# Performance work log

Measured on AMD Instinct MI355X. Metric: run time of the kernel, lower is better.

## Reference

```python
import jax, jax.numpy as jnp
import numpy as np

B, S, HID = 2, 2048, 1024
NH, HD = 4, 256
SCALE = HD ** -0.5


def _rope(x, fr, fi):
    # x: [B,S,NH,HD]; fr/fi: [S,HD//2]
    b, s, n, d = x.shape
    xr = x.reshape(b, s, n, d // 2, 2)
    re, im = xr[..., 0], xr[..., 1]
    fr = fr[None, :, None, :]
    fi = fi[None, :, None, :]
    rr = re * fr - im * fi
    ri = re * fi + im * fr
    return jnp.stack((rr, ri), axis=-1).reshape(b, s, n, d)


def setup_inputs() -> dict:
    key = jax.random.key(0)
    k1, k2, k3 = jax.random.split(key, 3)
    hidden_states = jax.random.normal(k1, (B, S, HID), dtype=jnp.float32)
    # RoPE frequencies (standard theta=10000)
    inv_freq = 1.0 / (10000.0 ** (np.arange(0, HD, 2, dtype=np.float32) / HD))  # [HD//2]
    t = np.arange(S, dtype=np.float32)
    ang = np.outer(t, inv_freq)  # [S, HD//2]
    freqs_real = jnp.asarray(np.cos(ang), dtype=jnp.float32)
    freqs_imag = jnp.asarray(np.sin(ang), dtype=jnp.float32)
    # causal additive mask [1,1,S,S]
    causal = jnp.tril(jnp.ones((S, S), dtype=bool))
    mask = jnp.where(causal, 0.0, -1e9).astype(jnp.float32)[None, None]
    W_qkv = jax.random.normal(k2, (3 * HID, HID), dtype=jnp.float32) * (HID ** -0.5)
    W_o = jax.random.normal(k3, (HID, HID), dtype=jnp.float32) * (HID ** -0.5)
    return {"hidden_states": hidden_states, "freqs_real": freqs_real,
            "freqs_imag": freqs_imag, "mask": mask, "W_qkv": W_qkv, "W_o": W_o}


def reference(hidden_states, freqs_real, freqs_imag, mask, W_qkv, W_o):
    b, s, _ = hidden_states.shape
    qkv = hidden_states @ W_qkv.T  # [B,S,3*HID]
    qkv = qkv.reshape(b, s, 3, NH, HD)
    q, k, v = qkv[:, :, 0], qkv[:, :, 1], qkv[:, :, 2]
    q = _rope(q, freqs_real, freqs_imag)
    k = _rope(k, freqs_real, freqs_imag)
    scores = jnp.einsum('bqhd,bkhd->bhqk', q * SCALE, k) + mask  # [B,NH,S,S]
    probs = jax.nn.softmax(scores, axis=-1)
    attn = jnp.einsum('bhqk,bkhd->bqhd', probs, v).reshape(b, s, HID)
    return attn @ W_o.T
```

## Files before the change

### kernel.cpp

```cpp
#include <hip/hip_runtime.h>
#include <stdint.h>

#define NB 2
#define NS 2048
#define NHID 1024
#define NHEADS 4
#define DHEAD 256
#define NP 128
#define QK_SCALE 0.0625f

typedef unsigned short ushort_t;
typedef __bf16 bf16x8 __attribute__((ext_vector_type(8)));
typedef float floatx4 __attribute__((ext_vector_type(4)));
typedef short shortx8 __attribute__((ext_vector_type(8)));
typedef unsigned short ushortx4 __attribute__((ext_vector_type(4)));
typedef unsigned short ushortx8 __attribute__((ext_vector_type(8)));

__device__ __forceinline__ float bf2f(ushort_t u) {
    unsigned int x = ((unsigned int)u) << 16;
    return __builtin_bit_cast(float, x);
}
__device__ __forceinline__ ushort_t f2bf(float f) {
    unsigned int u = __builtin_bit_cast(unsigned int, f);
    u += 0x7fff + ((u >> 16) & 1);
    return (ushort_t)(u >> 16);
}

__device__ __forceinline__ floatx4 mfma16(bf16x8 a, bf16x8 b, floatx4 c) {
    return __builtin_amdgcn_mfma_f32_16x16x32_bf16(a, b, c, 0, 0, 0);
}

__device__ __forceinline__ void gload_lds16(const void* g, void* l) {
    __builtin_amdgcn_global_load_lds(
        (const __attribute__((address_space(1))) void*)g,
        (__attribute__((address_space(3))) void*)l, 16, 0, 0);
}

#define N4_H (4096 * 1024 / 4)
#define N4_WQ (3072 * 1024 / 4)
#define N4_WO (1024 * 1024 / 4)
__global__ __launch_bounds__(256) void cast3_kernel(const float* __restrict__ inH,
                                                    const float* __restrict__ inWq,
                                                    const float* __restrict__ inWo,
                                                    ushort_t* __restrict__ out) {
    int i = blockIdx.x * 256 + threadIdx.x;
    const float* src;
    int j = i;
    if (i < N4_H) {
        src = inH;
    } else if (i < N4_H + N4_WQ) {
        src = inWq; j = i - N4_H;
    } else {
        src = inWo; j = i - (N4_H + N4_WQ);
    }
    float4 v = ((const float4*)src)[j];
    ushortx4 o = { f2bf(v.x), f2bf(v.y), f2bf(v.z), f2bf(v.w) };
    ((ushortx4*)out)[i] = o;
}


__global__ __launch_bounds__(256) void gemm_bt_f32s(const ushort_t* __restrict__ A,
                                                    const ushort_t* __restrict__ Bt,
                                                    float* __restrict__ C0,
                                                    float* __restrict__ C1,
                                                    int M, int N, int K) {
    __shared__ ushort_t sA[128 * 64];
    __shared__ ushort_t sB[128 * 64];
    const int t = threadIdx.x;
    const int m0 = blockIdx.y * 128;
    const int n0 = blockIdx.x * 128;
    const int kz = blockIdx.z;
    float* Cout = kz ? C1 : C0;
    const int kbeg = kz * (K / 2), kend = kbeg + K / 2;
    const int w = t >> 6, l = t & 63;
    const int wm = (w >> 1) * 64, wn = (w & 1) * 64;
    const int lc = l & 15, lq = l >> 4;

    floatx4 acc[4][4];
#pragma unroll
    for (int i = 0; i < 4; i++)
#pragma unroll
        for (int j = 0; j < 4; j++) acc[i][j] = (floatx4){0.f, 0.f, 0.f, 0.f};

    const int srow = w * 8 + (l >> 3);
    const int scol = ((((l & 7) - (l >> 3)) & 7)) * 8;
    const ushort_t* Ag = A + (size_t)(m0 + srow) * K + scol;
    const ushort_t* Bg = Bt + (size_t)(n0 + srow) * K + scol;
    ushort_t* lA = &sA[(size_t)t * 8];
    ushort_t* lB = &sB[(size_t)t * 8];

    for (int kk = kbeg; kk < kend; kk += 64) {
        __syncthreads();
#pragma unroll
        for (int j = 0; j < 4; j++) {
            gload_lds16(Ag + kk + (size_t)j * 32 * K, lA + j * 2048);
            gload_lds16(Bg + kk + (size_t)j * 32 * K, lB + j * 2048);
        }
        __syncthreads();
#pragma unroll
        for (int ks = 0; ks < 2; ks++) {
            bf16x8 af[4], bfv[4];
#pragma unroll
            for (int i = 0; i < 4; i++) {
                int R = wm + i * 16 + lc;
                af[i] = *(const bf16x8*)&sA[R * 64 + ((ks * 4 + lq + R) & 7) * 8];
            }
#pragma unroll
            for (int j = 0; j < 4; j++) {
                int R = wn + j * 16 + lc;
                bfv[j] = *(const bf16x8*)&sB[R * 64 + ((ks * 4 + lq + R) & 7) * 8];
            }
#pragma unroll
            for (int i = 0; i < 4; i++)
#pragma unroll
                for (int j = 0; j < 4; j++)
                    acc[i][j] = mfma16(af[i], bfv[j], acc[i][j]);
        }
    }

#pragma unroll
    for (int i = 0; i < 4; i++) {
        int row = m0 + wm + i * 16 + lq * 4;
#pragma unroll
        for (int j = 0; j < 4; j++) {
            int col = n0 + wn + j * 16 + lc;
#pragma unroll
            for (int r = 0; r < 4; r++)
                Cout[(size_t)(row + r) * N + col] = acc[i][j][r];
        }
    }
}

__global__ __launch_bounds__(256) void add_f32(const float* __restrict__ a,
                                               const float* __restrict__ b,
                                               float* __restrict__ o, int n4) {
    int i = blockIdx.x * 256 + threadIdx.x;
    if (i < n4) {
        float4 x = ((const float4*)a)[i];
        float4 y = ((const float4*)b)[i];
        float4 z = { x.x + y.x, x.y + y.y, x.z + y.z, x.w + y.w };
        ((float4*)o)[i] = z;
    }
}

__global__ __launch_bounds__(256) void gemm_qkv(const ushort_t* __restrict__ A,
                                                const ushort_t* __restrict__ Bt,
                                                const float* __restrict__ fre,
                                                const float* __restrict__ fim,
                                                ushort_t* __restrict__ Q,
                                                ushort_t* __restrict__ Kk,
                                                ushort_t* __restrict__ Vt) {
    const int M_K = 1024;
    __shared__ ushort_t sA[128 * 64];
    __shared__ ushort_t sB[128 * 64];
    const int t = threadIdx.x;
    const int m0 = blockIdx.y * 128;
    const int n0 = blockIdx.x * 128;
    const int w = t >> 6, l = t & 63;
    const int wm = (w >> 1) * 64, wn = (w & 1) * 64;
    const int lc = l & 15, lq = l >> 4;

    floatx4 acc[4][4];
#pragma unroll
    for (int i = 0; i < 4; i++)
#pragma unroll
        for (int j = 0; j < 4; j++) acc[i][j] = (floatx4){0.f, 0.f, 0.f, 0.f};

    const int srow = w * 8 + (l >> 3);
    const int scol = ((((l & 7) - (l >> 3)) & 7)) * 8;
    const ushort_t* Ag = A + (size_t)(m0 + srow) * M_K + scol;
    const ushort_t* Bg = Bt + (size_t)(n0 + srow) * M_K + scol;
    ushort_t* lA = &sA[(size_t)t * 8];
    ushort_t* lB = &sB[(size_t)t * 8];

    for (int kk = 0; kk < M_K; kk += 64) {
        __syncthreads();
#pragma unroll
        for (int j = 0; j < 4; j++) {
            gload_lds16(Ag + kk + (size_t)j * 32 * M_K, lA + j * 2048);
            gload_lds16(Bg + kk + (size_t)j * 32 * M_K, lB + j * 2048);
        }
        __syncthreads();
#pragma unroll
        for (int ks = 0; ks < 2; ks++) {
            bf16x8 af[4], bfv[4];
#pragma unroll
            for (int i = 0; i < 4; i++) {
                int R = wm + i * 16 + lc;
                af[i] = *(const bf16x8*)&sA[R * 64 + ((ks * 4 + lq + R) & 7) * 8];
            }
#pragma unroll
            for (int j = 0; j < 4; j++) {
                int R = wn + j * 16 + lc;
                bfv[j] = *(const bf16x8*)&sB[R * 64 + ((ks * 4 + lq + R) & 7) * 8];
            }
#pragma unroll
            for (int i = 0; i < 4; i++)
#pragma unroll
                for (int j = 0; j < 4; j++)
                    acc[i][j] = mfma16(af[i], bfv[j], acc[i][j]);
        }
    }

    const int sect = n0 >> 10;
#pragma unroll
    for (int i = 0; i < 4; i++) {
        int row = m0 + wm + i * 16 + lq * 4;
        int b = row >> 11;
        int srow2 = row & 2047;
#pragma unroll
        for (int j = 0; j < 4; j++) {
            int col = n0 + wn + j * 16 + lc;
            int d = col & 255;
            int h = (col >> 8) & 3;
            int bh = b * NHEADS + h;
            if (sect == 2) {
                ushortx4 pack = { f2bf(acc[i][j][0]), f2bf(acc[i][j][1]),
                                  f2bf(acc[i][j][2]), f2bf(acc[i][j][3]) };
                *(ushortx4*)&Vt[((size_t)bh * 256 + d) * NS + srow2] = pack;
            } else {
                int p = d >> 1;
                int odd = d & 1;
                ushort_t* dst = (sect == 0) ? Q : Kk;
#pragma unroll
                for (int r = 0; r < 4; r++) {
                    float v = acc[i][j][r];
                    float vp = __shfl_xor(v, 1);
                    int s = srow2 + r;
                    float c = fre[s * NP + p], si = fim[s * NP + p];
                    float out = odd ? (vp * si + v * c) : (v * c - vp * si);
                    if (sect == 0) out *= QK_SCALE;
                    dst[((size_t)bh * NS + s) * DHEAD + d] = f2bf(out);
                }
            }
        }
    }
}

#define BQ3 128
#define BKV3 64
#define PPAD 72
#define CHCAP 6
#define NPART_BH 51
#define OPART_SPLIT 224

__global__ __launch_bounds__(256, 2) void flash_attn4(const ushort_t* __restrict__ Q,
                                                      const ushort_t* __restrict__ K,
                                                      const ushort_t* __restrict__ Vt,
                                                      ushort_t* __restrict__ OpA,
                                                      ushort_t* __restrict__ OpB,
                                                      float* __restrict__ ml) {
    __shared__ ushort_t sK[BKV3 * 256];
    __shared__ ushort_t sV[DHEAD * 64];
    __shared__ ushort_t sP[4][16 * PPAD];

    int rem = blockIdx.x, qt = 15, nsp;
    for (;;) {
        nsp = (2 * (qt + 1) + CHCAP - 1) / CHCAP;
        if (rem < nsp) break;
        rem -= nsp;
        qt--;
    }
    const int nch = 2 * (qt + 1);
    const int cbeg = rem * CHCAP;
    const int cend = (cbeg + CHCAP < nch) ? cbeg + CHCAP : nch;

    const int h = blockIdx.y, b = blockIdx.z;
    const int t = threadIdx.x, w = t >> 6, l = t & 63;
    const int lc = l & 15, lq = l >> 4;
    const int bh = b * NHEADS + h;
    const size_t base = (size_t)bh * NS * DHEAD;
    const int q0 = qt * BQ3;

    const int krb = w * 2 + (l >> 5);
    const int kck = ((l & 31) - (krb & 7)) & 31;
    const size_t koff = (size_t)krb * 256 + kck * 8;
    const int vrb = w * 8 + (l >> 3);
    const int vck = ((l & 7) - (vrb & 7)) & 7;
    const size_t voff = (size_t)vrb * NS + vck * 8;
    ushort_t* dK = &sK[w * 512 + l * 8];
    ushort_t* dV = &sV[w * 512 + l * 8];

    bf16x8 qf[2][8];
#pragma unroll
    for (int gq = 0; gq < 2; gq++) {
        const ushort_t* qrow = Q + base + (size_t)(q0 + w * 32 + gq * 16 + lc) * DHEAD + lq * 8;
#pragma unroll
        for (int dk = 0; dk < 8; dk++) qf[gq][dk] = *(const bf16x8*)(qrow + dk * 32);
    }

    floatx4 accO[2][16];
#pragma unroll
    for (int gq = 0; gq < 2; gq++)
#pragma unroll
        for (int j = 0; j < 16; j++) accO[gq][j] = (floatx4){0.f, 0.f, 0.f, 0.f};
    float lrun[2][4] = {{0.f, 0.f, 0.f, 0.f}, {0.f, 0.f, 0.f, 0.f}};

    for (int kc = cbeg; kc < cend; kc++) {
        const int kb = kc * BKV3;
        __syncthreads();
        {
            const ushort_t* ksrc = K + base + (size_t)kb * 256 + koff;
            const ushort_t* vsrc = Vt + base + kb + voff;
#pragma unroll
            for (int j = 0; j < 8; j++)
                gload_lds16(ksrc + j * (8 * 256), dK + j * 2048);
#pragma unroll
            for (int j = 0; j < 8; j++)
                gload_lds16(vsrc + j * (32 * NS), dV + j * 2048);
        }
        __syncthreads();

        floatx4 sfr[2][4];
#pragma unroll
        for (int gq = 0; gq < 2; gq++)
#pragma unroll
            for (int g = 0; g < 4; g++) sfr[gq][g] = (floatx4){0.f, 0.f, 0.f, 0.f};
#pragma unroll
        for (int dk = 0; dk < 8; dk++) {
#pragma unroll
            for (int g = 0; g < 4; g++) {
                int R = g * 16 + lc;
                int phys = (dk * 4 + lq + (R & 7)) & 31;
                bf16x8 bk = *(const bf16x8*)&sK[R * 256 + phys * 8];
                sfr[0][g] = mfma16(qf[0][dk], bk, sfr[0][g]);
                sfr[1][g] = mfma16(qf[1][dk], bk, sfr[1][g]);
            }
        }

        if (kc >= nch - 2) {
#pragma unroll
            for (int gq = 0; gq < 2; gq++)
#pragma unroll
                for (int g = 0; g < 4; g++) {
                    int kg = kb + g * 16 + lc;
                    int qr = q0 + w * 32 + gq * 16 + lq * 4;
#pragma unroll
                    for (int r = 0; r < 4; r++)
                        if (kg > qr + r) sfr[gq][g][r] = -1e30f;
                }
        }

        ushort_t* pw = sP[w];
#pragma unroll
        for (int gq = 0; gq < 2; gq++) {
#pragma unroll
            for (int g = 0; g < 4; g++)
#pragma unroll
                for (int r = 0; r < 4; r++) {
                    float p = __expf(sfr[gq][g][r]);
                    lrun[gq][r] += p;
                    pw[(lq * 4 + r) * PPAD + g * 16 + lc] = f2bf(p);
                }
            bf16x8 ap0 = *(const bf16x8*)&pw[lc * PPAD + lq * 8];
            bf16x8 ap1 = *(const bf16x8*)&pw[lc * PPAD + 32 + lq * 8];
#pragma unroll
            for (int j = 0; j < 16; j++) {
                int D = j * 16 + lc;
                int ph0 = (lq + (D & 7)) & 7;
                int ph1 = (4 + lq + (D & 7)) & 7;
                bf16x8 bv0 = *(const bf16x8*)&sV[D * 64 + ph0 * 8];
                bf16x8 bv1 = *(const bf16x8*)&sV[D * 64 + ph1 * 8];
                accO[gq][j] = mfma16(ap0, bv0, accO[gq][j]);
                accO[gq][j] = mfma16(ap1, bv1, accO[gq][j]);
            }
        }
    }

    const int pid = bh * NPART_BH + blockIdx.x;
    ushort_t* op = (pid < OPART_SPLIT) ? OpA + (size_t)pid * (128 * 256)
                                       : OpB + (size_t)(pid - OPART_SPLIT) * (128 * 256);
#pragma unroll
    for (int gq = 0; gq < 2; gq++) {
#pragma unroll
        for (int r = 0; r < 4; r++) {
            int row = w * 32 + gq * 16 + lq * 4 + r;
#pragma unroll
            for (int j = 0; j < 16; j++)
                op[row * 256 + j * 16 + lc] = f2bf(accO[gq][j][r]);
            float lv = lrun[gq][r];
#pragma unroll
            for (int off = 1; off < 16; off <<= 1) lv += __shfl_xor(lv, off);
            if (lc == 0) ml[(size_t)pid * 128 + row] = lv;
        }
    }
}

__global__ __launch_bounds__(256) void combine_parts2(const ushort_t* __restrict__ OpA,
                                                      const ushort_t* __restrict__ OpB,
                                                      const float* __restrict__ ml,
                                                      ushort_t* __restrict__ O) {
    const int qt = blockIdx.x >> 3, rsub = blockIdx.x & 7;
    const int h = blockIdx.y, b = blockIdx.z;
    const int bh = b * NHEADS + h;
    int bbase = 0;
    for (int q = 15; q > qt; q--) bbase += (2 * (q + 1) + CHCAP - 1) / CHCAP;
    const int nsp = (2 * (qt + 1) + CHCAP - 1) / CHCAP;
    const int pid0 = bh * NPART_BH + bbase;

    const int t = threadIdx.x;
    const int rl = t >> 4;
    const int c0 = (t & 15) * 16;
    const int row = rsub * 16 + rl;

    float so[16];
#pragma unroll
    for (int k = 0; k < 16; k++) so[k] = 0.f;
    float sl = 0.f;

    for (int i = 0; i < nsp; i++) {
        int pid = pid0 + i;
        const ushort_t* op = (pid < OPART_SPLIT)
                                 ? OpA + (size_t)pid * (128 * 256)
                                 : OpB + (size_t)(pid - OPART_SPLIT) * (128 * 256);
        const ushort_t* p = op + row * 256 + c0;
        ushortx8 a0 = *(const ushortx8*)p;
        ushortx8 a1 = *(const ushortx8*)(p + 8);
#pragma unroll
        for (int k = 0; k < 8; k++) {
            so[k] += bf2f(a0[k]);
            so[8 + k] += bf2f(a1[k]);
        }
        sl += ml[(size_t)pid * 128 + row];
    }

    float inv = 1.f / sl;
    ushortx8 o0, o1;
#pragma unroll
    for (int k = 0; k < 8; k++) {
        o0[k] = f2bf(so[k] * inv);
        o1[k] = f2bf(so[8 + k] * inv);
    }
    int s = qt * BQ3 + row;
    ushort_t* dst = O + ((size_t)(b * NS + s) * NHEADS + h) * DHEAD + c0;
    *(ushortx8*)dst = o0;
    *(ushortx8*)(dst + 8) = o1;
}

extern "C" void kernel_launch(void* const* d_in, const int* in_sizes, int n_in,
                              void* d_out, int out_size, void* d_ws, size_t ws_size,
                              hipStream_t stream) {
    const float* hidden = (const float*)d_in[0];
    const float* fre = (const float*)d_in[1];
    const float* fim = (const float*)d_in[2];
    const float* Wqkv = (const float*)d_in[4];
    const float* Wo = (const float*)d_in[5];

    char* ws = (char*)d_ws;
    ushort_t* hb    = (ushort_t*)(ws);
    ushort_t* wqkvb = (ushort_t*)(ws + 8388608);
    ushort_t* wob   = (ushort_t*)(ws + 14680064);
    ushort_t* qb    = (ushort_t*)(ws + 16777216);
    ushort_t* kb    = (ushort_t*)(ws + 25165824);
    ushort_t* vtb   = (ushort_t*)(ws + 33554432);
    ushort_t* OpA   = (ushort_t*)(ws);
    ushort_t* OpB   = (ushort_t*)(ws + 41943040);
    ushort_t* oattn = (ushort_t*)(ws + 16777216);
    float*    gP0   = (float*)(ws + 25165824);
    float*    gP1   = (float*)(ws + 41943040);
    float*    ml    = (float*)(ws + 58720256);

    cast3_kernel<<<(N4_H + N4_WQ + N4_WO) / 256, 256, 0, stream>>>(hidden, Wqkv, Wo, hb);

    gemm_qkv<<<dim3(3072 / 128, 4096 / 128), 256, 0, stream>>>(
        hb, wqkvb, fre, fim, qb, kb, vtb);

    flash_attn4<<<dim3(NPART_BH, NHEADS, NB), 256, 0, stream>>>(qb, kb, vtb, OpA, OpB, ml);
    combine_parts2<<<dim3(128, NHEADS, NB), 256, 0, stream>>>(OpA, OpB, ml, oattn);

    gemm_bt_f32s<<<dim3(1024 / 128, 4096 / 128, 2), 256, 0, stream>>>(
        oattn, wob, gP0, gP1, 4096, 1024, 1024);
    add_f32<<<4096, 256, 0, stream>>>(gP0, gP1, (float*)d_out, 4096 * 1024 / 4);
}
```

Before: 208.6 us.

## Replace split-K output GEMM with 128x64 tiles and batch P·V over query groups

The output projection no longer splits K into two halves that write separate fp32 partial buffers and then need an add kernel. It now uses 128x64 tiles over the full K and writes directly to the output, which keeps the block count at 512 and drops one launch plus the partial-buffer traffic. In the attention kernel, the P tile for both 16-row query groups is stored in a swizzled 32x64 LDS layout, so each V fragment is loaded once and reused for both groups. This halves V reads from LDS, at the cost of more live registers and a longer K loop per GEMM block.

```diff
diff --git a/kernel.cpp b/kernel.cpp
--- a/kernel.cpp
+++ b/kernel.cpp
@@ -59,61 +59,60 @@
 }
 
 
-__global__ __launch_bounds__(256) void gemm_bt_f32s(const ushort_t* __restrict__ A,
+__global__ __launch_bounds__(256) void gemm_bt_f32n(const ushort_t* __restrict__ A,
                                                     const ushort_t* __restrict__ Bt,
-                                                    float* __restrict__ C0,
-                                                    float* __restrict__ C1,
+                                                    float* __restrict__ Cout,
                                                     int M, int N, int K) {
     __shared__ ushort_t sA[128 * 64];
-    __shared__ ushort_t sB[128 * 64];
+    __shared__ ushort_t sB[64 * 64];
     const int t = threadIdx.x;
     const int m0 = blockIdx.y * 128;
-    const int n0 = blockIdx.x * 128;
-    const int kz = blockIdx.z;
-    float* Cout = kz ? C1 : C0;
-    const int kbeg = kz * (K / 2), kend = kbeg + K / 2;
+    const int n0 = blockIdx.x * 64;
     const int w = t >> 6, l = t & 63;
-    const int wm = (w >> 1) * 64, wn = (w & 1) * 64;
+    const int wm = (w >> 1) * 64, wn = (w & 1) * 32;
     const int lc = l & 15, lq = l >> 4;
 
-    floatx4 acc[4][4];
+    floatx4 acc[4][2];
 #pragma unroll
     for (int i = 0; i < 4; i++)
 #pragma unroll
-        for (int j = 0; j < 4; j++) acc[i][j] = (floatx4){0.f, 0.f, 0.f, 0.f};
-
-    const int srow = w * 8 + (l >> 3);
-    const int scol = ((((l & 7) - (l >> 3)) & 7)) * 8;
-    const ushort_t* Ag = A + (size_t)(m0 + srow) * K + scol;
-    const ushort_t* Bg = Bt + (size_t)(n0 + srow) * K + scol;
+        for (int j = 0; j < 2; j++) acc[i][j] = (floatx4){0.f, 0.f, 0.f, 0.f};
+
+    const int arow = w * 8 + (l >> 3);
+    const int acol = (((l & 7) - (l >> 3)) & 7) * 8;
+    const ushort_t* Ag = A + (size_t)(m0 + arow) * K + acol;
     ushort_t* lA = &sA[(size_t)t * 8];
+    const int brow = t >> 3;
+    const int bcol = (((t & 7) - ((t >> 3) & 7)) & 7) * 8;
+    const ushort_t* Bg = Bt + (size_t)(n0 + brow) * K + bcol;
     ushort_t* lB = &sB[(size_t)t * 8];
 
-    for (int kk = kbeg; kk < kend; kk += 64) {
-        __syncthreads();
-#pragma unroll
-        for (int j = 0; j < 4; j++) {
+    for (int kk = 0; kk < K; kk += 64) {
+        __syncthreads();
+#pragma unroll
+        for (int j = 0; j < 4; j++)
             gload_lds16(Ag + kk + (size_t)j * 32 * K, lA + j * 2048);
+#pragma unroll
+        for (int j = 0; j < 2; j++)
             gload_lds16(Bg + kk + (size_t)j * 32 * K, lB + j * 2048);
-        }
         __syncthreads();
 #pragma unroll
         for (int ks = 0; ks < 2; ks++) {
-            bf16x8 af[4], bfv[4];
+            bf16x8 af[4], bfv[2];
 #pragma unroll
             for (int i = 0; i < 4; i++) {
                 int R = wm + i * 16 + lc;
                 af[i] = *(const bf16x8*)&sA[R * 64 + ((ks * 4 + lq + R) & 7) * 8];
             }
 #pragma unroll
-            for (int j = 0; j < 4; j++) {
+            for (int j = 0; j < 2; j++) {
                 int R = wn + j * 16 + lc;
                 bfv[j] = *(const bf16x8*)&sB[R * 64 + ((ks * 4 + lq + R) & 7) * 8];
             }
 #pragma unroll
             for (int i = 0; i < 4; i++)
 #pragma unroll
-                for (int j = 0; j < 4; j++)
+                for (int j = 0; j < 2; j++)
                     acc[i][j] = mfma16(af[i], bfv[j], acc[i][j]);
         }
     }
@@ -122,24 +121,12 @@
     for (int i = 0; i < 4; i++) {
         int row = m0 + wm + i * 16 + lq * 4;
 #pragma unroll
-        for (int j = 0; j < 4; j++) {
+        for (int j = 0; j < 2; j++) {
             int col = n0 + wn + j * 16 + lc;
 #pragma unroll
             for (int r = 0; r < 4; r++)
                 Cout[(size_t)(row + r) * N + col] = acc[i][j][r];
         }
-    }
-}
-
-__global__ __launch_bounds__(256) void add_f32(const float* __restrict__ a,
-                                               const float* __restrict__ b,
-                                               float* __restrict__ o, int n4) {
-    int i = blockIdx.x * 256 + threadIdx.x;
-    if (i < n4) {
-        float4 x = ((const float4*)a)[i];
-        float4 y = ((const float4*)b)[i];
-        float4 z = { x.x + y.x, x.y + y.y, x.z + y.z, x.w + y.w };
-        ((float4*)o)[i] = z;
     }
 }
 
@@ -239,20 +226,19 @@
 
 #define BQ3 128
 #define BKV3 64
-#define PPAD 72
 #define CHCAP 6
 #define NPART_BH 51
 #define OPART_SPLIT 224
 
-__global__ __launch_bounds__(256, 2) void flash_attn4(const ushort_t* __restrict__ Q,
-                                                      const ushort_t* __restrict__ K,
-                                                      const ushort_t* __restrict__ Vt,
-                                                      ushort_t* __restrict__ OpA,
-                                                      ushort_t* __restrict__ OpB,
-                                                      float* __restrict__ ml) {
+__global__ __launch_bounds__(256, 2) void flash_attn4b(const ushort_t* __restrict__ Q,
+                                                       const ushort_t* __restrict__ K,
+                                                       const ushort_t* __restrict__ Vt,
+                                                       ushort_t* __restrict__ OpA,
+                                                       ushort_t* __restrict__ OpB,
+                                                       float* __restrict__ ml) {
     __shared__ ushort_t sK[BKV3 * 256];
     __shared__ ushort_t sV[DHEAD * 64];
-    __shared__ ushort_t sP[4][16 * PPAD];
+    __shared__ ushort_t sP[4][32 * 64];
 
     int rem = blockIdx.x, qt = 15, nsp;
     for (;;) {
@@ -343,27 +329,35 @@
 
         ushort_t* pw = sP[w];
 #pragma unroll
-        for (int gq = 0; gq < 2; gq++) {
+        for (int gq = 0; gq < 2; gq++)
 #pragma unroll
             for (int g = 0; g < 4; g++)
 #pragma unroll
                 for (int r = 0; r < 4; r++) {
                     float p = __expf(sfr[gq][g][r]);
                     lrun[gq][r] += p;
-                    pw[(lq * 4 + r) * PPAD + g * 16 + lc] = f2bf(p);
+                    int prow = gq * 16 + lq * 4 + r;
+                    int pcol = g * 16 + lc;
+                    pw[prow * 64 + (((pcol >> 3) + prow) & 7) * 8 + (pcol & 7)] = f2bf(p);
                 }
-            bf16x8 ap0 = *(const bf16x8*)&pw[lc * PPAD + lq * 8];
-            bf16x8 ap1 = *(const bf16x8*)&pw[lc * PPAD + 32 + lq * 8];
-#pragma unroll
-            for (int j = 0; j < 16; j++) {
-                int D = j * 16 + lc;
-                int ph0 = (lq + (D & 7)) & 7;
-                int ph1 = (4 + lq + (D & 7)) & 7;
-                bf16x8 bv0 = *(const bf16x8*)&sV[D * 64 + ph0 * 8];
-                bf16x8 bv1 = *(const bf16x8*)&sV[D * 64 + ph1 * 8];
-                accO[gq][j] = mfma16(ap0, bv0, accO[gq][j]);
-                accO[gq][j] = mfma16(ap1, bv1, accO[gq][j]);
-            }
+        bf16x8 ap[2][2];
+#pragma unroll
+        for (int gq = 0; gq < 2; gq++) {
+            int prow = gq * 16 + lc;
+            ap[gq][0] = *(const bf16x8*)&pw[prow * 64 + ((lq + prow) & 7) * 8];
+            ap[gq][1] = *(const bf16x8*)&pw[prow * 64 + ((lq + 4 + prow) & 7) * 8];
+        }
+#pragma unroll
+        for (int j = 0; j < 16; j++) {
+            int D = j * 16 + lc;
+            int ph0 = (lq + (D & 7)) & 7;
+            int ph1 = (4 + lq + (D & 7)) & 7;
+            bf16x8 bv0 = *(const bf16x8*)&sV[D * 64 + ph0 * 8];
+            bf16x8 bv1 = *(const bf16x8*)&sV[D * 64 + ph1 * 8];
+            accO[0][j] = mfma16(ap[0][0], bv0, accO[0][j]);
+            accO[0][j] = mfma16(ap[0][1], bv1, accO[0][j]);
+            accO[1][j] = mfma16(ap[1][0], bv0, accO[1][j]);
+            accO[1][j] = mfma16(ap[1][1], bv1, accO[1][j]);
         }
     }
 
@@ -456,8 +450,6 @@
     ushort_t* OpA   = (ushort_t*)(ws);
     ushort_t* OpB   = (ushort_t*)(ws + 41943040);
     ushort_t* oattn = (ushort_t*)(ws + 16777216);
-    float*    gP0   = (float*)(ws + 25165824);
-    float*    gP1   = (float*)(ws + 41943040);
     float*    ml    = (float*)(ws + 58720256);
 
     cast3_kernel<<<(N4_H + N4_WQ + N4_WO) / 256, 256, 0, stream>>>(hidden, Wqkv, Wo, hb);
@@ -465,10 +457,9 @@
     gemm_qkv<<<dim3(3072 / 128, 4096 / 128), 256, 0, stream>>>(
         hb, wqkvb, fre, fim, qb, kb, vtb);
 
-    flash_attn4<<<dim3(NPART_BH, NHEADS, NB), 256, 0, stream>>>(qb, kb, vtb, OpA, OpB, ml);
+    flash_attn4b<<<dim3(NPART_BH, NHEADS, NB), 256, 0, stream>>>(qb, kb, vtb, OpA, OpB, ml);
     combine_parts2<<<dim3(128, NHEADS, NB), 256, 0, stream>>>(OpA, OpB, ml, oattn);
 
-    gemm_bt_f32s<<<dim3(1024 / 128, 4096 / 128, 2), 256, 0, stream>>>(
-        oattn, wob, gP0, gP1, 4096, 1024, 1024);
-    add_f32<<<4096, 256, 0, stream>>>(gP0, gP1, (float*)d_out, 4096 * 1024 / 4);
-}
+    gemm_bt_f32n<<<dim3(1024 / 64, 4096 / 128), 256, 0, stream>>>(
+        oattn, wob, (float*)d_out, 4096, 1024, 1024);
+}
```

After: 237.9 us. +14.1%, slower.
